# Performance work log

Hardware: AMD Instinct MI355X
Metric: run time of the kernel (lower is better)

The kernel has to match this reference:

```python
import jax, jax.numpy as jnp
import numpy as np

B, T, U, D = 2, 512, 48, 512
H, K = 1024, 128  # hidden_channels, num_classes; fc1 in = 2*D = 1024


def setup_inputs() -> dict:
    key = jax.random.key(0)
    ks = jax.random.split(key, 9)
    s = 0.02
    return {
        "img_feature": jax.random.normal(ks[0], (B, T, D), jnp.float32),
        "label_feature": jax.random.normal(ks[1], (B, U, D), jnp.float32),
        "masks": jnp.ones((B, 1, T), jnp.float32),
        "W1": jax.random.normal(ks[2], (H, 2 * D), jnp.float32) * s,
        "b1": jnp.zeros((H,), jnp.float32),
        "W2": jax.random.normal(ks[3], (K, H), jnp.float32) * s,
        "b2": jnp.zeros((K,), jnp.float32),
        "conv_w": jax.random.normal(ks[4], (K, D), jnp.float32) * s,
        "conv_b": jnp.zeros((K,), jnp.float32),
    }


def reference(img_feature, label_feature, masks, W1, b1, W2, b2, conv_w, conv_b):
    # pointwise Conv1d over img features: (B,T,D) -> (B,K,T), masked
    img_seg_score = (jnp.einsum('btd,kd->bkt', img_feature, conv_w)
                     + conv_b[None, :, None]) * masks
    # fc1(cat(label, img)) == label @ Wl^T + img @ Wi^T + b1 (broadcast add),
    # avoiding the O(B*U*T*2D) repeat+cat intermediate.
    d = label_feature.shape[-1]
    Wl, Wi = W1[:, :d], W1[:, d:]
    lab = jnp.einsum('bud,hd->buh', label_feature, Wl)  # (B,U,H)
    img = jnp.einsum('btd,hd->bth', img_feature, Wi)    # (B,T,H)
    h = jnp.tanh(lab[:, :, None, :] + img[:, None, :, :] + b1)  # (B,U,T,H)
    joint = jnp.einsum('buth,kh->butk', h, W2) + b2
    joint_score = jax.nn.log_softmax(joint, axis=-1)
    return (img_seg_score, joint_score)
```

## Files before the change

kernel.cpp:

```cpp
#include <hip/hip_runtime.h>
#include <math.h>

#define BB 2
#define TT 512
#define UU 48
#define DD 512
#define HH 1024
#define KK 128

typedef __bf16 bf16x8 __attribute__((ext_vector_type(8)));
typedef float floatx4 __attribute__((ext_vector_type(4)));

__device__ __forceinline__ float fast_tanh(float x) {
    float e = __expf(2.0f * x);
    return __fdividef(e - 1.0f, e + 1.0f);
}

__global__ __launch_bounds__(256) void prep_kernel(
    const float* __restrict__ img, const float* __restrict__ labf,
    const float* __restrict__ W1, const float* __restrict__ W2,
    const float* __restrict__ conv_w,
    __bf16* __restrict__ img_b, __bf16* __restrict__ lab_b,
    __bf16* __restrict__ W1s_l, __bf16* __restrict__ W1s_i,
    __bf16* __restrict__ W2s, __bf16* __restrict__ cws) {
    int idx = blockIdx.x * 256 + threadIdx.x;
    if (idx < 524288) {
        img_b[idx] = (__bf16)img[idx];
    } else if (idx < 573440) {
        int i = idx - 524288;
        lab_b[i] = (__bf16)labf[i];
    } else if (idx < 1622016) {
        int i = idx - 573440;
        int half = i >> 19;
        int rr = i & 524287;
        int h = rr >> 9, d = rr & 511;
        float v = W1[(size_t)h * 1024 + half * 512 + d];
        __bf16* dst = half ? W1s_i : W1s_l;
        dst[(d >> 3) * (HH * 8) + h * 8 + (d & 7)] = (__bf16)v;
    } else if (idx < 1753088) {
        int i = idx - 1622016;
        int k = i >> 10, h = i & 1023;
        W2s[(h >> 3) * (KK * 8) + k * 8 + (h & 7)] = (__bf16)W2[i];
    } else if (idx < 1818624) {
        int i = idx - 1753088;
        int k = i >> 9, d = i & 511;
        cws[(d >> 3) * (KK * 8) + k * 8 + (d & 7)] = (__bf16)conv_w[i];
    }
}

__global__ __launch_bounds__(256) void mid_kernel(
    const __bf16* __restrict__ img_b, const __bf16* __restrict__ lab_b,
    const __bf16* __restrict__ W1s_l, const __bf16* __restrict__ W1s_i,
    const __bf16* __restrict__ cws,
    const float* __restrict__ b1, const float* __restrict__ conv_b,
    const float* __restrict__ masks,
    float* __restrict__ imgH, float* __restrict__ labH,
    float* __restrict__ seg_out) {
    __shared__ __align__(16) __bf16 a_s[32][72];
    __shared__ __align__(16) __bf16 w_s[8192];
    int bid = blockIdx.x;
    int tid = threadIdx.x;
    const __bf16* A;
    const __bf16* Ws;
    int r0, n0b, nout, region;
    if (bid < 256) {
        region = 0; A = img_b; Ws = W1s_i;
        r0 = (bid & 31) * 32; n0b = (bid >> 5) * 128; nout = HH;
    } else if (bid < 280) {
        region = 1; A = lab_b; Ws = W1s_l;
        int i = bid - 256; r0 = (i % 3) * 32; n0b = (i / 3) * 128; nout = HH;
    } else {
        region = 2; A = img_b; Ws = cws;
        r0 = (bid - 280) * 32; n0b = 0; nout = KK;
    }
    int lane = tid & 63, wv = tid >> 6;
    int m0 = (wv & 1) * 16, n0w = (wv >> 1) * 64;
    int q = lane >> 4, r = lane & 15;
    int arow = tid >> 3, acol = (tid & 7) * 8;
    floatx4 acc[4] = {};
    for (int c = 0; c < 8; ++c) {
        int cb = c * 64;
        *(bf16x8*)&a_s[arow][acol] =
            *(const bf16x8*)&A[(size_t)(r0 + arow) * DD + cb + acol];
        int cg = cb >> 3;
#pragma unroll
        for (int i2 = 0; i2 < 4; ++i2) {
            int uu = i2 * 256 + tid;
            int g = uu >> 7, j = uu & 127;
            *(bf16x8*)&w_s[uu * 8] =
                *(const bf16x8*)&Ws[((size_t)(cg + g) * nout + n0b + j) * 8];
        }
        __syncthreads();
#pragma unroll
        for (int kt = 0; kt < 2; ++kt) {
            bf16x8 af = *(const bf16x8*)&a_s[m0 + r][kt * 32 + q * 8];
#pragma unroll
            for (int nt = 0; nt < 4; ++nt) {
                bf16x8 bf = *(const bf16x8*)
                    &w_s[((kt * 4 + q) * 128 + n0w + nt * 16 + r) * 8];
                acc[nt] = __builtin_amdgcn_mfma_f32_16x16x32_bf16(
                    af, bf, acc[nt], 0, 0, 0);
            }
        }
        __syncthreads();
    }
    if (region == 0) {
#pragma unroll
        for (int nt = 0; nt < 4; ++nt) {
            int n = n0b + n0w + nt * 16 + r;
#pragma unroll
            for (int rr = 0; rr < 4; ++rr)
                imgH[(size_t)(r0 + m0 + 4 * q + rr) * HH + n] = acc[nt][rr];
        }
    } else if (region == 1) {
#pragma unroll
        for (int nt = 0; nt < 4; ++nt) {
            int n = n0b + n0w + nt * 16 + r;
            float bv = b1[n];
#pragma unroll
            for (int rr = 0; rr < 4; ++rr)
                labH[(size_t)(r0 + m0 + 4 * q + rr) * HH + n] = acc[nt][rr] + bv;
        }
    } else {
#pragma unroll
        for (int nt = 0; nt < 4; ++nt) {
            int k = n0w + nt * 16 + r;
            float bv = conv_b[k];
#pragma unroll
            for (int rr = 0; rr < 4; ++rr) {
                int row = r0 + m0 + 4 * q + rr;
                int b = row >> 9, t = row & 511;
                seg_out[((size_t)b * KK + k) * TT + t] =
                    (acc[nt][rr] + bv) * masks[row];
            }
        }
    }
}

__global__ __launch_bounds__(256) void joint_kernel2(
    const float* __restrict__ imgH,
    const float* __restrict__ labH,
    const __bf16* __restrict__ W2s,
    const float* __restrict__ b2,
    float* __restrict__ out) {
    __shared__ __align__(16) __bf16 h_s[64][72];
    __shared__ __align__(16) __bf16 w_s[8192];
    int tid = threadIdx.x;
    int bid = blockIdx.x;
    int t0 = (bid & 7) * 64;
    int rest = bid >> 3;
    int u = rest % UU;
    int b = rest / UU;
    const float* imgrow = imgH + ((size_t)b * TT + t0) * HH;
    const float* labrow = labH + ((size_t)b * UU + u) * HH;
    int lane = tid & 63, wv = tid >> 6;
    int m0 = wv * 16;
    int q = lane >> 4, r = lane & 15;
    int srow2 = (tid >> 3) * 2;
    int scol = (tid & 7) * 8;
    floatx4 acc[8] = {};
    for (int c = 0; c < 16; ++c) {
        int cb = c * 64;
        const __bf16* wsrc = W2s + (size_t)cb * KK;
#pragma unroll
        for (int i2 = 0; i2 < 4; ++i2) {
            int e = (i2 * 256 + tid) * 8;
            *(bf16x8*)&w_s[e] = *(const bf16x8*)&wsrc[e];
        }
        float lv[8];
        *(float4*)&lv[0] = *(const float4*)&labrow[cb + scol];
        *(float4*)&lv[4] = *(const float4*)&labrow[cb + scol + 4];
#pragma unroll
        for (int rr = 0; rr < 2; ++rr) {
            const float* ip = &imgrow[(size_t)(srow2 + rr) * HH + cb + scol];
            float4 iv0 = *(const float4*)ip;
            float4 iv1 = *(const float4*)(ip + 4);
            bf16x8 hv;
            hv[0] = (__bf16)fast_tanh(iv0.x + lv[0]);
            hv[1] = (__bf16)fast_tanh(iv0.y + lv[1]);
            hv[2] = (__bf16)fast_tanh(iv0.z + lv[2]);
            hv[3] = (__bf16)fast_tanh(iv0.w + lv[3]);
            hv[4] = (__bf16)fast_tanh(iv1.x + lv[4]);
            hv[5] = (__bf16)fast_tanh(iv1.y + lv[5]);
            hv[6] = (__bf16)fast_tanh(iv1.z + lv[6]);
            hv[7] = (__bf16)fast_tanh(iv1.w + lv[7]);
            *(bf16x8*)&h_s[srow2 + rr][scol] = hv;
        }
        __syncthreads();
#pragma unroll
        for (int kt = 0; kt < 2; ++kt) {
            bf16x8 af = *(const bf16x8*)&h_s[m0 + r][kt * 32 + q * 8];
#pragma unroll
            for (int nt = 0; nt < 8; ++nt) {
                bf16x8 bf = *(const bf16x8*)
                    &w_s[((kt * 4 + q) * 128 + nt * 16 + r) * 8];
                acc[nt] = __builtin_amdgcn_mfma_f32_16x16x32_bf16(
                    af, bf, acc[nt], 0, 0, 0);
            }
        }
        __syncthreads();
    }
    float b2v[8];
#pragma unroll
    for (int nt = 0; nt < 8; ++nt) b2v[nt] = b2[nt * 16 + r];
    float* orow = out + (((size_t)b * UU + u) * TT + t0 + m0) * KK;
#pragma unroll
    for (int rr = 0; rr < 4; ++rr) {
        float v[8];
        float mx = -INFINITY;
#pragma unroll
        for (int nt = 0; nt < 8; ++nt) {
            v[nt] = acc[nt][rr] + b2v[nt];
            mx = fmaxf(mx, v[nt]);
        }
        mx = fmaxf(mx, __shfl_xor(mx, 1, 16));
        mx = fmaxf(mx, __shfl_xor(mx, 2, 16));
        mx = fmaxf(mx, __shfl_xor(mx, 4, 16));
        mx = fmaxf(mx, __shfl_xor(mx, 8, 16));
        float s = 0.f;
#pragma unroll
        for (int nt = 0; nt < 8; ++nt) s += __expf(v[nt] - mx);
        s += __shfl_xor(s, 1, 16);
        s += __shfl_xor(s, 2, 16);
        s += __shfl_xor(s, 4, 16);
        s += __shfl_xor(s, 8, 16);
        float lse = mx + __logf(s);
        int row = 4 * q + rr;
#pragma unroll
        for (int nt = 0; nt < 8; ++nt)
            orow[(size_t)row * KK + nt * 16 + r] = v[nt] - lse;
    }
}

extern "C" void kernel_launch(void* const* d_in, const int* in_sizes, int n_in,
                              void* d_out, int out_size, void* d_ws, size_t ws_size,
                              hipStream_t stream) {
    const float* img    = (const float*)d_in[0];
    const float* labf   = (const float*)d_in[1];
    const float* masks  = (const float*)d_in[2];
    const float* W1     = (const float*)d_in[3];
    const float* b1     = (const float*)d_in[4];
    const float* W2     = (const float*)d_in[5];
    const float* b2     = (const float*)d_in[6];
    const float* conv_w = (const float*)d_in[7];
    const float* conv_b = (const float*)d_in[8];
    float* out = (float*)d_out;
    float* ws = (float*)d_ws;

    float* imgH = ws;
    float* labH = imgH + 1024 * 1024;
    __bf16* base  = (__bf16*)(labH + 96 * 1024);
    __bf16* img_b = base;
    __bf16* lab_b = img_b + 524288;
    __bf16* W1s_l = lab_b + 49152;
    __bf16* W1s_i = W1s_l + 524288;
    __bf16* W2s   = W1s_i + 524288;
    __bf16* cws   = W2s + 131072;

    prep_kernel<<<7104, 256, 0, stream>>>(img, labf, W1, W2, conv_w,
                                          img_b, lab_b, W1s_l, W1s_i, W2s, cws);
    mid_kernel<<<312, 256, 0, stream>>>(img_b, lab_b, W1s_l, W1s_i, cws,
                                        b1, conv_b, masks, imgH, labH, out);
    joint_kernel2<<<768, 256, 0, stream>>>(imgH, labH, W2s, b2,
                                           out + (size_t)BB * KK * TT);
}
```

Measured before the change: 144.6 us.

## Fuse bf16 conversion into GEMM loads, bf16 intermediates, double-buffer joint kernel

Removes the separate prep kernel: the mid kernel now reads fp32 inputs and weights directly and converts them to bf16 while staging into shared memory, and extra blocks relayout W2. The img/label projections are stored as bf16, which halves intermediate traffic into the joint kernel. The joint kernel double-buffers its shared tiles with register prefetch, dropping one barrier per iteration, and sets launch bounds for 3 blocks per CU. tanh moves from an exp/divide form to a clamped rational approximation. This adds precision risk from the bf16 intermediates and the tanh approximation, and the mid kernel's W1 reads are now strided and uncoalesced.

```diff
diff --git a/kernel.cpp b/kernel.cpp
--- a/kernel.cpp
+++ b/kernel.cpp
@@ -11,67 +11,47 @@
 typedef __bf16 bf16x8 __attribute__((ext_vector_type(8)));
 typedef float floatx4 __attribute__((ext_vector_type(4)));
 
-__device__ __forceinline__ float fast_tanh(float x) {
-    float e = __expf(2.0f * x);
-    return __fdividef(e - 1.0f, e + 1.0f);
-}
-
-__global__ __launch_bounds__(256) void prep_kernel(
+__device__ __forceinline__ float tanh_fast(float x) {
+    float x2 = x * x;
+    float num = x * fmaf(x2, x2 + 105.0f, 945.0f);
+    float den = fmaf(x2, fmaf(x2, 15.0f, 420.0f), 945.0f);
+    float r = num * __fdividef(1.0f, den);
+    return fminf(1.0f, fmaxf(-1.0f, r));
+}
+
+__global__ __launch_bounds__(256) void mid_kernel2(
     const float* __restrict__ img, const float* __restrict__ labf,
     const float* __restrict__ W1, const float* __restrict__ W2,
     const float* __restrict__ conv_w,
-    __bf16* __restrict__ img_b, __bf16* __restrict__ lab_b,
-    __bf16* __restrict__ W1s_l, __bf16* __restrict__ W1s_i,
-    __bf16* __restrict__ W2s, __bf16* __restrict__ cws) {
-    int idx = blockIdx.x * 256 + threadIdx.x;
-    if (idx < 524288) {
-        img_b[idx] = (__bf16)img[idx];
-    } else if (idx < 573440) {
-        int i = idx - 524288;
-        lab_b[i] = (__bf16)labf[i];
-    } else if (idx < 1622016) {
-        int i = idx - 573440;
-        int half = i >> 19;
-        int rr = i & 524287;
-        int h = rr >> 9, d = rr & 511;
-        float v = W1[(size_t)h * 1024 + half * 512 + d];
-        __bf16* dst = half ? W1s_i : W1s_l;
-        dst[(d >> 3) * (HH * 8) + h * 8 + (d & 7)] = (__bf16)v;
-    } else if (idx < 1753088) {
-        int i = idx - 1622016;
-        int k = i >> 10, h = i & 1023;
-        W2s[(h >> 3) * (KK * 8) + k * 8 + (h & 7)] = (__bf16)W2[i];
-    } else if (idx < 1818624) {
-        int i = idx - 1753088;
-        int k = i >> 9, d = i & 511;
-        cws[(d >> 3) * (KK * 8) + k * 8 + (d & 7)] = (__bf16)conv_w[i];
-    }
-}
-
-__global__ __launch_bounds__(256) void mid_kernel(
-    const __bf16* __restrict__ img_b, const __bf16* __restrict__ lab_b,
-    const __bf16* __restrict__ W1s_l, const __bf16* __restrict__ W1s_i,
-    const __bf16* __restrict__ cws,
     const float* __restrict__ b1, const float* __restrict__ conv_b,
     const float* __restrict__ masks,
-    float* __restrict__ imgH, float* __restrict__ labH,
-    float* __restrict__ seg_out) {
+    __bf16* __restrict__ imgHb, __bf16* __restrict__ labHb,
+    __bf16* __restrict__ W2s, float* __restrict__ seg_out) {
+    int bid = blockIdx.x, tid = threadIdx.x;
+    if (bid >= 312) {
+        int base = (bid - 312) * 256 + tid;
+#pragma unroll
+        for (int i = 0; i < 32; ++i) {
+            int o = base + i * 4096;
+            int hg = o >> 10, kk2 = (o >> 3) & 127, hl = o & 7;
+            W2s[o] = (__bf16)W2[(size_t)kk2 * HH + hg * 8 + hl];
+        }
+        return;
+    }
     __shared__ __align__(16) __bf16 a_s[32][72];
     __shared__ __align__(16) __bf16 w_s[8192];
-    int bid = blockIdx.x;
-    int tid = threadIdx.x;
-    const __bf16* A;
-    const __bf16* Ws;
-    int r0, n0b, nout, region;
+    const float* Arow;
+    const float* Wbase;
+    int r0, n0b, wstride, region;
     if (bid < 256) {
-        region = 0; A = img_b; Ws = W1s_i;
-        r0 = (bid & 31) * 32; n0b = (bid >> 5) * 128; nout = HH;
+        region = 0; Arow = img; Wbase = W1 + 512; wstride = 1024;
+        r0 = (bid & 31) * 32; n0b = (bid >> 5) * 128;
     } else if (bid < 280) {
-        region = 1; A = lab_b; Ws = W1s_l;
-        int i = bid - 256; r0 = (i % 3) * 32; n0b = (i / 3) * 128; nout = HH;
+        region = 1; Arow = labf; Wbase = W1; wstride = 1024;
+        int i = bid - 256; r0 = (i % 3) * 32; n0b = (i / 3) * 128;
     } else {
-        region = 2; A = img_b; Ws = cws;
-        r0 = (bid - 280) * 32; n0b = 0; nout = KK;
+        region = 2; Arow = img; Wbase = conv_w; wstride = 512;
+        r0 = (bid - 280) * 32; n0b = 0;
     }
     int lane = tid & 63, wv = tid >> 6;
     int m0 = (wv & 1) * 16, n0w = (wv >> 1) * 64;
@@ -80,15 +60,30 @@
     floatx4 acc[4] = {};
     for (int c = 0; c < 8; ++c) {
         int cb = c * 64;
-        *(bf16x8*)&a_s[arow][acol] =
-            *(const bf16x8*)&A[(size_t)(r0 + arow) * DD + cb + acol];
-        int cg = cb >> 3;
+        {
+            const float* ap = &Arow[(size_t)(r0 + arow) * DD + cb + acol];
+            float4 a0 = *(const float4*)ap;
+            float4 a1 = *(const float4*)(ap + 4);
+            bf16x8 av;
+            av[0] = (__bf16)a0.x; av[1] = (__bf16)a0.y;
+            av[2] = (__bf16)a0.z; av[3] = (__bf16)a0.w;
+            av[4] = (__bf16)a1.x; av[5] = (__bf16)a1.y;
+            av[6] = (__bf16)a1.z; av[7] = (__bf16)a1.w;
+            *(bf16x8*)&a_s[arow][acol] = av;
+        }
 #pragma unroll
         for (int i2 = 0; i2 < 4; ++i2) {
-            int uu = i2 * 256 + tid;
-            int g = uu >> 7, j = uu & 127;
-            *(bf16x8*)&w_s[uu * 8] =
-                *(const bf16x8*)&Ws[((size_t)(cg + g) * nout + n0b + j) * 8];
+            int g = i2 * 256 + tid;
+            int kg = g >> 7, n = g & 127;
+            const float* wp = &Wbase[(size_t)(n0b + n) * wstride + cb + kg * 8];
+            float4 w0 = *(const float4*)wp;
+            float4 w1 = *(const float4*)(wp + 4);
+            bf16x8 wvv;
+            wvv[0] = (__bf16)w0.x; wvv[1] = (__bf16)w0.y;
+            wvv[2] = (__bf16)w0.z; wvv[3] = (__bf16)w0.w;
+            wvv[4] = (__bf16)w1.x; wvv[5] = (__bf16)w1.y;
+            wvv[6] = (__bf16)w1.z; wvv[7] = (__bf16)w1.w;
+            *(bf16x8*)&w_s[g * 8] = wvv;
         }
         __syncthreads();
 #pragma unroll
@@ -96,10 +91,10 @@
             bf16x8 af = *(const bf16x8*)&a_s[m0 + r][kt * 32 + q * 8];
 #pragma unroll
             for (int nt = 0; nt < 4; ++nt) {
-                bf16x8 bf = *(const bf16x8*)
+                bf16x8 bfv = *(const bf16x8*)
                     &w_s[((kt * 4 + q) * 128 + n0w + nt * 16 + r) * 8];
                 acc[nt] = __builtin_amdgcn_mfma_f32_16x16x32_bf16(
-                    af, bf, acc[nt], 0, 0, 0);
+                    af, bfv, acc[nt], 0, 0, 0);
             }
         }
         __syncthreads();
@@ -110,7 +105,8 @@
             int n = n0b + n0w + nt * 16 + r;
 #pragma unroll
             for (int rr = 0; rr < 4; ++rr)
-                imgH[(size_t)(r0 + m0 + 4 * q + rr) * HH + n] = acc[nt][rr];
+                imgHb[(size_t)(r0 + m0 + 4 * q + rr) * HH + n] =
+                    (__bf16)acc[nt][rr];
         }
     } else if (region == 1) {
 #pragma unroll
@@ -119,7 +115,8 @@
             float bv = b1[n];
 #pragma unroll
             for (int rr = 0; rr < 4; ++rr)
-                labH[(size_t)(r0 + m0 + 4 * q + rr) * HH + n] = acc[nt][rr] + bv;
+                labHb[(size_t)(r0 + m0 + 4 * q + rr) * HH + n] =
+                    (__bf16)(acc[nt][rr] + bv);
         }
     } else {
 #pragma unroll
@@ -137,68 +134,76 @@
     }
 }
 
-__global__ __launch_bounds__(256) void joint_kernel2(
-    const float* __restrict__ imgH,
-    const float* __restrict__ labH,
+__global__ __launch_bounds__(256, 3) void joint_kernel3(
+    const __bf16* __restrict__ imgHb,
+    const __bf16* __restrict__ labHb,
     const __bf16* __restrict__ W2s,
     const float* __restrict__ b2,
     float* __restrict__ out) {
-    __shared__ __align__(16) __bf16 h_s[64][72];
-    __shared__ __align__(16) __bf16 w_s[8192];
-    int tid = threadIdx.x;
-    int bid = blockIdx.x;
+    __shared__ __align__(16) __bf16 h_s[2][64][72];
+    __shared__ __align__(16) __bf16 w_s[2][8192];
+    int tid = threadIdx.x, bid = blockIdx.x;
     int t0 = (bid & 7) * 64;
     int rest = bid >> 3;
-    int u = rest % UU;
-    int b = rest / UU;
-    const float* imgrow = imgH + ((size_t)b * TT + t0) * HH;
-    const float* labrow = labH + ((size_t)b * UU + u) * HH;
+    int u = rest % UU, b = rest / UU;
+    const __bf16* imgrow = imgHb + ((size_t)b * TT + t0) * HH;
+    const __bf16* labrow = labHb + ((size_t)b * UU + u) * HH;
     int lane = tid & 63, wv = tid >> 6;
     int m0 = wv * 16;
     int q = lane >> 4, r = lane & 15;
-    int srow2 = (tid >> 3) * 2;
-    int scol = (tid & 7) * 8;
+    int srow2 = (tid >> 3) * 2, scol = (tid & 7) * 8;
     floatx4 acc[8] = {};
+    bf16x8 iv0, iv1, lv, wr0, wr1, wr2, wr3;
+    {
+        iv0 = *(const bf16x8*)&imgrow[(size_t)srow2 * HH + scol];
+        iv1 = *(const bf16x8*)&imgrow[(size_t)(srow2 + 1) * HH + scol];
+        lv  = *(const bf16x8*)&labrow[scol];
+        wr0 = *(const bf16x8*)&W2s[(0 * 256 + tid) * 8];
+        wr1 = *(const bf16x8*)&W2s[(1 * 256 + tid) * 8];
+        wr2 = *(const bf16x8*)&W2s[(2 * 256 + tid) * 8];
+        wr3 = *(const bf16x8*)&W2s[(3 * 256 + tid) * 8];
+    }
+#pragma unroll 2
     for (int c = 0; c < 16; ++c) {
-        int cb = c * 64;
-        const __bf16* wsrc = W2s + (size_t)cb * KK;
-#pragma unroll
-        for (int i2 = 0; i2 < 4; ++i2) {
-            int e = (i2 * 256 + tid) * 8;
-            *(bf16x8*)&w_s[e] = *(const bf16x8*)&wsrc[e];
-        }
-        float lv[8];
-        *(float4*)&lv[0] = *(const float4*)&labrow[cb + scol];
-        *(float4*)&lv[4] = *(const float4*)&labrow[cb + scol + 4];
-#pragma unroll
-        for (int rr = 0; rr < 2; ++rr) {
-            const float* ip = &imgrow[(size_t)(srow2 + rr) * HH + cb + scol];
-            float4 iv0 = *(const float4*)ip;
-            float4 iv1 = *(const float4*)(ip + 4);
-            bf16x8 hv;
-            hv[0] = (__bf16)fast_tanh(iv0.x + lv[0]);
-            hv[1] = (__bf16)fast_tanh(iv0.y + lv[1]);
-            hv[2] = (__bf16)fast_tanh(iv0.z + lv[2]);
-            hv[3] = (__bf16)fast_tanh(iv0.w + lv[3]);
-            hv[4] = (__bf16)fast_tanh(iv1.x + lv[4]);
-            hv[5] = (__bf16)fast_tanh(iv1.y + lv[5]);
-            hv[6] = (__bf16)fast_tanh(iv1.z + lv[6]);
-            hv[7] = (__bf16)fast_tanh(iv1.w + lv[7]);
-            *(bf16x8*)&h_s[srow2 + rr][scol] = hv;
+        int buf = c & 1;
+        *(bf16x8*)&w_s[buf][(0 * 256 + tid) * 8] = wr0;
+        *(bf16x8*)&w_s[buf][(1 * 256 + tid) * 8] = wr1;
+        *(bf16x8*)&w_s[buf][(2 * 256 + tid) * 8] = wr2;
+        *(bf16x8*)&w_s[buf][(3 * 256 + tid) * 8] = wr3;
+        {
+            bf16x8 h0, h1;
+#pragma unroll
+            for (int i = 0; i < 8; ++i) {
+                float xl = (float)lv[i];
+                h0[i] = (__bf16)tanh_fast((float)iv0[i] + xl);
+                h1[i] = (__bf16)tanh_fast((float)iv1[i] + xl);
+            }
+            *(bf16x8*)&h_s[buf][srow2][scol] = h0;
+            *(bf16x8*)&h_s[buf][srow2 + 1][scol] = h1;
         }
         __syncthreads();
+        if (c < 15) {
+            int cb = (c + 1) * 64;
+            iv0 = *(const bf16x8*)&imgrow[(size_t)srow2 * HH + cb + scol];
+            iv1 = *(const bf16x8*)&imgrow[(size_t)(srow2 + 1) * HH + cb + scol];
+            lv  = *(const bf16x8*)&labrow[cb + scol];
+            const __bf16* wsrc = W2s + (size_t)cb * KK;
+            wr0 = *(const bf16x8*)&wsrc[(0 * 256 + tid) * 8];
+            wr1 = *(const bf16x8*)&wsrc[(1 * 256 + tid) * 8];
+            wr2 = *(const bf16x8*)&wsrc[(2 * 256 + tid) * 8];
+            wr3 = *(const bf16x8*)&wsrc[(3 * 256 + tid) * 8];
+        }
 #pragma unroll
         for (int kt = 0; kt < 2; ++kt) {
-            bf16x8 af = *(const bf16x8*)&h_s[m0 + r][kt * 32 + q * 8];
+            bf16x8 af = *(const bf16x8*)&h_s[buf][m0 + r][kt * 32 + q * 8];
 #pragma unroll
             for (int nt = 0; nt < 8; ++nt) {
-                bf16x8 bf = *(const bf16x8*)
-                    &w_s[((kt * 4 + q) * 128 + nt * 16 + r) * 8];
+                bf16x8 bfv = *(const bf16x8*)
+                    &w_s[buf][((kt * 4 + q) * 128 + nt * 16 + r) * 8];
                 acc[nt] = __builtin_amdgcn_mfma_f32_16x16x32_bf16(
-                    af, bf, acc[nt], 0, 0, 0);
-            }
-        }
-        __syncthreads();
+                    af, bfv, acc[nt], 0, 0, 0);
+            }
+        }
     }
     float b2v[8];
 #pragma unroll
@@ -245,22 +250,15 @@
     const float* conv_w = (const float*)d_in[7];
     const float* conv_b = (const float*)d_in[8];
     float* out = (float*)d_out;
-    float* ws = (float*)d_ws;
-
-    float* imgH = ws;
-    float* labH = imgH + 1024 * 1024;
-    __bf16* base  = (__bf16*)(labH + 96 * 1024);
-    __bf16* img_b = base;
-    __bf16* lab_b = img_b + 524288;
-    __bf16* W1s_l = lab_b + 49152;
-    __bf16* W1s_i = W1s_l + 524288;
-    __bf16* W2s   = W1s_i + 524288;
-    __bf16* cws   = W2s + 131072;
-
-    prep_kernel<<<7104, 256, 0, stream>>>(img, labf, W1, W2, conv_w,
-                                          img_b, lab_b, W1s_l, W1s_i, W2s, cws);
-    mid_kernel<<<312, 256, 0, stream>>>(img_b, lab_b, W1s_l, W1s_i, cws,
-                                        b1, conv_b, masks, imgH, labH, out);
-    joint_kernel2<<<768, 256, 0, stream>>>(imgH, labH, W2s, b2,
+
+    __bf16* base   = (__bf16*)d_ws;
+    __bf16* imgHb  = base;
+    __bf16* labHb  = imgHb + 1024 * 1024;
+    __bf16* W2s    = labHb + 96 * 1024;
+
+    mid_kernel2<<<328, 256, 0, stream>>>(img, labf, W1, W2, conv_w,
+                                         b1, conv_b, masks,
+                                         imgHb, labHb, W2s, out);
+    joint_kernel3<<<768, 256, 0, stream>>>(imgHb, labHb, W2s, b2,
                                            out + (size_t)BB * KK * TT);
 }
```

After: 147.9 us. +2.3%, slower.
